# Optimization experiments

Hardware: AMD Instinct MI355X
Metric: run time of the kernel (lower is better)

Reference implementation:

```python
import math
import jax, jax.numpy as jnp
import numpy as np

# --- dimensions ---
B = 32          # crystals
N_PER = 96      # building blocks per crystal
M = B * N_PER   # total nodes = 3072
H = 8           # no_heads
CH = 16         # c_hidden
PQK = 8         # no_qk_points
PV = 12         # no_v_points
CS = 256        # c_s
CZ = 128        # c_z
E = B * N_PER * N_PER  # dense intra-crystal edges = 294912
INV_SOFTPLUS_1 = 0.541324854612918


def _quat_to_rot(q):
    """Unit quaternion [M,4] -> rotation matrices [M,3,3]."""
    w, x, y, z = q[:, 0], q[:, 1], q[:, 2], q[:, 3]
    R = jnp.stack([
        1 - 2 * (y * y + z * z), 2 * (x * y - w * z), 2 * (x * z + w * y),
        2 * (x * y + w * z), 1 - 2 * (x * x + z * z), 2 * (y * z - w * x),
        2 * (x * z - w * y), 2 * (y * z + w * x), 1 - 2 * (x * x + y * y)],
        axis=-1)
    return R.reshape(-1, 3, 3)


def _lin_params(k, din, dout):
    kw, kb = jax.random.split(k)
    W = jax.random.normal(kw, (din, dout), jnp.float32) / np.sqrt(din).astype(np.float32)
    b = jax.random.normal(kb, (dout,), jnp.float32) * 0.01
    return W, b


def setup_inputs() -> dict:
    key = jax.random.key(0)
    ks = jax.random.split(key, 16)
    s = jax.random.normal(ks[0], (M, CS), jnp.float32)
    z = jax.random.normal(ks[1], (E, CZ), jnp.float32)
    quat = jax.random.normal(ks[2], (M, 4), jnp.float32)
    rot = _quat_to_rot(quat / jnp.linalg.norm(quat, axis=-1, keepdims=True))
    trans = jax.random.normal(ks[3], (M, 3), jnp.float32)
    L = jax.random.normal(ks[4], (B, 6), jnp.float32)
    # block-diagonal fully-connected intra-crystal edges
    i = np.repeat(np.arange(N_PER), N_PER)
    j = np.tile(np.arange(N_PER), N_PER)
    off = (np.arange(B) * N_PER)[:, None]
    src = (off + i[None, :]).reshape(-1)
    tgt = (off + j[None, :]).reshape(-1)
    edge_index = jnp.asarray(np.stack([src, tgt]), jnp.int32)
    num_bbs = jnp.full((B,), N_PER, jnp.int32)
    Wq, bq = _lin_params(ks[5], CS, H * CH)
    Wkv, bkv = _lin_params(ks[6], CS, 2 * H * CH)
    Wqp, bqp = _lin_params(ks[7], CS, H * PQK * 3)
    Wkvp, bkvp = _lin_params(ks[8], CS, H * (PQK + PV) * 3)
    Wb, bb = _lin_params(ks[9], CZ, H)
    Wl, bl = _lin_params(ks[10], 6, H)
    head_weights = INV_SOFTPLUS_1 + 0.1 * jax.random.normal(ks[11], (H,), jnp.float32)
    Wout, bout = _lin_params(ks[12], H * (CH + 3 * PV) + 6, CS)
    return dict(s=s, z=z, rot=rot, trans=trans, L=L,
                Wq=Wq, bq=bq, Wkv=Wkv, bkv=bkv, Wqp=Wqp, bqp=bqp,
                Wkvp=Wkvp, bkvp=bkvp, Wb=Wb, bb=bb, Wl=Wl, bl=bl,
                head_weights=head_weights, Wout=Wout, bout=bout,
                edge_index=edge_index, num_bbs=num_bbs)


def reference(s, z, rot, trans, L, Wq, bq, Wkv, bkv, Wqp, bqp, Wkvp, bkvp,
              Wb, bb, Wl, bl, head_weights, Wout, bout, edge_index, num_bbs):
    src, tgt = edge_index[0], edge_index[1]
    # scalar q/k/v
    q = (s @ Wq + bq).reshape(M, H, CH)
    kv = (s @ Wkv + bkv).reshape(M, H, 2 * CH)
    k, v = kv[..., :CH], kv[..., CH:]

    # point q/k/v: torch splits last dim into 3 coord chunks then stacks -> reshape (M,3,H,P)
    def points(W, bias, P):
        p = (s @ W + bias).reshape(M, 3, H, P).transpose(0, 2, 3, 1)  # [M,H,P,3]
        return jnp.einsum('mij,mhpj->mhpi', rot, p) + trans[:, None, None, :]

    q_pts = points(Wqp, bqp, PQK)                 # [M,H,PQK,3] in global frame
    kv_pts = points(Wkvp, bkvp, PQK + PV)         # [M,H,PQK+PV,3]
    k_pts, v_pts = kv_pts[:, :, :PQK], kv_pts[:, :, PQK:]

    b_pair = z @ Wb + bb                          # [E,H]
    batch_idx = jnp.repeat(jnp.arange(B), num_bbs, total_repeat_length=M)  # node -> crystal
    l_nodes = (L @ Wl + bl)[batch_idx]            # [M,H]

    # fused multi-term attention logits
    a = jnp.einsum('ehc,ehc->eh', q[tgt], k[src]) * math.sqrt(1.0 / (4 * CH))
    a = a + 0.5 * b_pair + 0.5 * l_nodes[src]
    disp = q_pts[tgt] - k_pts[src]                # [E,H,PQK,3]
    pt_att = jnp.sum(disp * disp, axis=-1)        # [E,H,PQK]
    hw = jax.nn.softplus(head_weights) * math.sqrt(1.0 / (4 * (PQK * 9.0 / 2)))
    a = a - 0.5 * jnp.sum(pt_att * hw[None, :, None], axis=-1)

    # segment softmax over incoming edges of each target node
    amax = jax.ops.segment_max(a, tgt, num_segments=M)
    ex = jnp.exp(a - amax[tgt])
    denom = jax.ops.segment_sum(ex, tgt, num_segments=M)
    attn = ex / denom[tgt]                        # [E,H]

    o = jax.ops.segment_sum(attn[..., None] * v[src], tgt, num_segments=M)
    o = o.reshape(M, H * CH)
    o_pt = jax.ops.segment_sum(attn[..., None, None] * v_pts[src], tgt, num_segments=M)
    o_pt = o_pt.reshape(M, H * PV, 3)
    o_l = L[batch_idx]                            # [M,6]
    o_feats = jnp.concatenate([o, o_pt[..., 0], o_pt[..., 1], o_pt[..., 2], o_l], axis=-1)
    return o_feats @ Wout + bout                  # [M,CS]
```

## Files before the change

kernel.cpp:

```cpp
#include <hip/hip_runtime.h>
#include <math.h>

#define B_    32
#define NPER_ 96
#define M_    3072
#define H_    8
#define CH_   16
#define PQK_  8
#define PV_   12
#define CS_   256
#define CZ_   128
#define E_    294912
#define NCAT_ 1056
#define OF_   432

template <bool ALIGN_A>
__global__ __launch_bounds__(256) void gemm64(const float* __restrict__ A,
                                              const float* __restrict__ W,
                                              const float* __restrict__ bias,
                                              float* __restrict__ C,
                                              int N, int K, int KW) {
  __shared__ float As[16][68];
  __shared__ float Bs[16][64];
  const int tid = threadIdx.x;
  const int tx = tid & 15, ty = tid >> 4;
  const int row0 = blockIdx.y * 64, col0 = blockIdx.x * 64;
  float acc[4][4] = {};

  for (int k0 = 0; k0 < K; k0 += 16) {
    {
      const int m = tid >> 2, k4 = (tid & 3) * 4;
      const int gk = k0 + k4;
      float a0 = 0.f, a1 = 0.f, a2 = 0.f, a3 = 0.f;
      if (ALIGN_A) {
        const float4 av = *reinterpret_cast<const float4*>(A + (size_t)(row0 + m) * K + gk);
        a0 = av.x; a1 = av.y; a2 = av.z; a3 = av.w;
      } else {
        const float* ap = A + (size_t)(row0 + m) * K;
        if (gk + 0 < K) a0 = ap[gk + 0];
        if (gk + 1 < K) a1 = ap[gk + 1];
        if (gk + 2 < K) a2 = ap[gk + 2];
        if (gk + 3 < K) a3 = ap[gk + 3];
      }
      As[k4 + 0][m] = a0; As[k4 + 1][m] = a1; As[k4 + 2][m] = a2; As[k4 + 3][m] = a3;
    }
    {
      const int kk = tid >> 4, n4 = (tid & 15) * 4;
      const int gk = k0 + kk, gn = col0 + n4;
      float4 bv; bv.x = 0.f; bv.y = 0.f; bv.z = 0.f; bv.w = 0.f;
      if (gk < KW) {
        if (gn + 3 < N) {
          bv = *reinterpret_cast<const float4*>(W + (size_t)gk * N + gn);
        } else {
          const float* wp = W + (size_t)gk * N;
          if (gn + 0 < N) bv.x = wp[gn + 0];
          if (gn + 1 < N) bv.y = wp[gn + 1];
          if (gn + 2 < N) bv.z = wp[gn + 2];
          if (gn + 3 < N) bv.w = wp[gn + 3];
        }
      }
      *reinterpret_cast<float4*>(&Bs[kk][n4]) = bv;
    }
    __syncthreads();
#pragma unroll
    for (int kk = 0; kk < 16; ++kk) {
      const float4 a_ = *reinterpret_cast<const float4*>(&As[kk][ty * 4]);
      const float4 b_ = *reinterpret_cast<const float4*>(&Bs[kk][tx * 4]);
      acc[0][0] += a_.x * b_.x; acc[0][1] += a_.x * b_.y; acc[0][2] += a_.x * b_.z; acc[0][3] += a_.x * b_.w;
      acc[1][0] += a_.y * b_.x; acc[1][1] += a_.y * b_.y; acc[1][2] += a_.y * b_.z; acc[1][3] += a_.y * b_.w;
      acc[2][0] += a_.z * b_.x; acc[2][1] += a_.z * b_.y; acc[2][2] += a_.z * b_.z; acc[2][3] += a_.z * b_.w;
      acc[3][0] += a_.w * b_.x; acc[3][1] += a_.w * b_.y; acc[3][2] += a_.w * b_.z; acc[3][3] += a_.w * b_.w;
    }
    __syncthreads();
  }
  const int gn0 = col0 + tx * 4;
#pragma unroll
  for (int i2 = 0; i2 < 4; ++i2) {
    const int gr = row0 + ty * 4 + i2;
    if (gn0 + 3 < N) {
      const float4 bsv = *reinterpret_cast<const float4*>(bias + gn0);
      float4 cv;
      cv.x = acc[i2][0] + bsv.x; cv.y = acc[i2][1] + bsv.y;
      cv.z = acc[i2][2] + bsv.z; cv.w = acc[i2][3] + bsv.w;
      *reinterpret_cast<float4*>(C + (size_t)gr * N + gn0) = cv;
    } else {
#pragma unroll
      for (int j2 = 0; j2 < 4; ++j2) {
        const int gn = gn0 + j2;
        if (gn < N) C[(size_t)gr * N + gn] = acc[i2][j2] + bias[gn];
      }
    }
  }
}

__global__ __launch_bounds__(256) void gemm128(const float* __restrict__ A,
                                               const float* __restrict__ W,
                                               const float* __restrict__ bias,
                                               float* __restrict__ C,
                                               int N, int K) {
  __shared__ float As[16][132];
  __shared__ float Bs[16][64];
  const int tid = threadIdx.x;
  const int tx = tid & 15, ty = tid >> 4;
  const int row0 = blockIdx.y * 128, col0 = blockIdx.x * 64;
  float acc[8][4] = {};

  for (int k0 = 0; k0 < K; k0 += 16) {
#pragma unroll
    for (int u = 0; u < 2; ++u) {
      const int idx = tid * 2 + u;
      const int r = idx >> 2, c = (idx & 3) * 4;
      const float4 av = *reinterpret_cast<const float4*>(A + (size_t)(row0 + r) * K + k0 + c);
      As[c + 0][r] = av.x; As[c + 1][r] = av.y; As[c + 2][r] = av.z; As[c + 3][r] = av.w;
    }
    {
      const int kk = tid >> 4, n4 = (tid & 15) * 4;
      const int gn = col0 + n4;
      float4 bv; bv.x = 0.f; bv.y = 0.f; bv.z = 0.f; bv.w = 0.f;
      if (gn + 3 < N) {
        bv = *reinterpret_cast<const float4*>(W + (size_t)(k0 + kk) * N + gn);
      } else {
        const float* wp = W + (size_t)(k0 + kk) * N;
        if (gn + 0 < N) bv.x = wp[gn + 0];
        if (gn + 1 < N) bv.y = wp[gn + 1];
        if (gn + 2 < N) bv.z = wp[gn + 2];
        if (gn + 3 < N) bv.w = wp[gn + 3];
      }
      *reinterpret_cast<float4*>(&Bs[kk][n4]) = bv;
    }
    __syncthreads();
#pragma unroll
    for (int kk = 0; kk < 16; ++kk) {
      const float4 a0 = *reinterpret_cast<const float4*>(&As[kk][ty * 8]);
      const float4 a1 = *reinterpret_cast<const float4*>(&As[kk][ty * 8 + 4]);
      const float4 b_ = *reinterpret_cast<const float4*>(&Bs[kk][tx * 4]);
      acc[0][0] += a0.x * b_.x; acc[0][1] += a0.x * b_.y; acc[0][2] += a0.x * b_.z; acc[0][3] += a0.x * b_.w;
      acc[1][0] += a0.y * b_.x; acc[1][1] += a0.y * b_.y; acc[1][2] += a0.y * b_.z; acc[1][3] += a0.y * b_.w;
      acc[2][0] += a0.z * b_.x; acc[2][1] += a0.z * b_.y; acc[2][2] += a0.z * b_.z; acc[2][3] += a0.z * b_.w;
      acc[3][0] += a0.w * b_.x; acc[3][1] += a0.w * b_.y; acc[3][2] += a0.w * b_.z; acc[3][3] += a0.w * b_.w;
      acc[4][0] += a1.x * b_.x; acc[4][1] += a1.x * b_.y; acc[4][2] += a1.x * b_.z; acc[4][3] += a1.x * b_.w;
      acc[5][0] += a1.y * b_.x; acc[5][1] += a1.y * b_.y; acc[5][2] += a1.y * b_.z; acc[5][3] += a1.y * b_.w;
      acc[6][0] += a1.z * b_.x; acc[6][1] += a1.z * b_.y; acc[6][2] += a1.z * b_.z; acc[6][3] += a1.z * b_.w;
      acc[7][0] += a1.w * b_.x; acc[7][1] += a1.w * b_.y; acc[7][2] += a1.w * b_.z; acc[7][3] += a1.w * b_.w;
    }
    __syncthreads();
  }
  const int gn0 = col0 + tx * 4;
#pragma unroll
  for (int i2 = 0; i2 < 8; ++i2) {
    const int gr = row0 + ty * 8 + i2;
    if (gn0 + 3 < N) {
      const float4 bsv = *reinterpret_cast<const float4*>(bias + gn0);
      float4 cv;
      cv.x = acc[i2][0] + bsv.x; cv.y = acc[i2][1] + bsv.y;
      cv.z = acc[i2][2] + bsv.z; cv.w = acc[i2][3] + bsv.w;
      *reinterpret_cast<float4*>(C + (size_t)gr * N + gn0) = cv;
    } else {
#pragma unroll
      for (int j2 = 0; j2 < 4; ++j2) {
        const int gn = gn0 + j2;
        if (gn < N) C[(size_t)gr * N + gn] = acc[i2][j2] + bias[gn];
      }
    }
  }
}

__global__ __launch_bounds__(256) void pack_w(const float* __restrict__ Wq,
                                              const float* __restrict__ Wkv,
                                              const float* __restrict__ Wqp,
                                              const float* __restrict__ Wkvp,
                                              const float* __restrict__ bq,
                                              const float* __restrict__ bkv,
                                              const float* __restrict__ bqp,
                                              const float* __restrict__ bkvp,
                                              float* __restrict__ Wcat,
                                              float* __restrict__ bcat) {
  const int t = blockIdx.x * 256 + threadIdx.x;
  if (t < 256 * NCAT_) {
    const int k = t / NCAT_, n = t - k * NCAT_;
    float v;
    if (n < 128)      v = Wq [k * 128 + n];
    else if (n < 384) v = Wkv[k * 256 + n - 128];
    else if (n < 576) v = Wqp[k * 192 + n - 384];
    else              v = Wkvp[k * 480 + n - 576];
    Wcat[t] = v;
  }
  if (t < NCAT_) {
    float v;
    if (t < 128)      v = bq[t];
    else if (t < 384) v = bkv[t - 128];
    else if (t < 576) v = bqp[t - 384];
    else              v = bkvp[t - 576];
    bcat[t] = v;
  }
}

__global__ __launch_bounds__(256) void rotate_pts(const float* __restrict__ praw,
                                                  const float* __restrict__ rot,
                                                  const float* __restrict__ trans,
                                                  const float* __restrict__ L,
                                                  float* __restrict__ qpts,
                                                  float* __restrict__ kpts,
                                                  float* __restrict__ vpts,
                                                  float* __restrict__ ofeat) {
  const int m = blockIdx.x;
  const int t = threadIdx.x;
  float R[9], T[3];
#pragma unroll
  for (int a = 0; a < 9; ++a) R[a] = rot[m * 9 + a];
#pragma unroll
  for (int a = 0; a < 3; ++a) T[a] = trans[m * 3 + a];
  const float* prow = praw + (size_t)m * NCAT_;

  if (t < 64) {
    const float x = prow[384 + t];
    const float y = prow[384 + 64 + t];
    const float z = prow[384 + 128 + t];
    const int h = t >> 3, p = t & 7;
    float* dst = qpts + ((size_t)(m * 8 + h) * 8 + p) * 3;
    dst[0] = R[0] * x + R[1] * y + R[2] * z + T[0];
    dst[1] = R[3] * x + R[4] * y + R[5] * z + T[1];
    dst[2] = R[6] * x + R[7] * y + R[8] * z + T[2];
  } else if (t < 224) {
    const int idx = t - 64;
    const float x = prow[576 + idx];
    const float y = prow[576 + 160 + idx];
    const float z = prow[576 + 320 + idx];
    const int h = idx / 20, p = idx % 20;
    const float o0 = R[0] * x + R[1] * y + R[2] * z + T[0];
    const float o1 = R[3] * x + R[4] * y + R[5] * z + T[1];
    const float o2 = R[6] * x + R[7] * y + R[8] * z + T[2];
    float* dst = (p < 8) ? (kpts + ((size_t)(m * 8 + h) * 8 + p) * 3)
                         : (vpts + ((size_t)(m * 8 + h) * 12 + (p - 8)) * 3);
    dst[0] = o0; dst[1] = o1; dst[2] = o2;
  } else if (t < 230) {
    ofeat[(size_t)m * OF_ + 416 + (t - 224)] = L[(m / NPER_) * 6 + (t - 224)];
  }
}

__global__ __launch_bounds__(256) void bpair_kernel(const float* __restrict__ z,
                                                    const float* __restrict__ Wb,
                                                    const float* __restrict__ bb,
                                                    float* __restrict__ bT2) {
  __shared__ float lds_out[96 * 9];
  const int bid = blockIdx.x;
  const int b = bid / 96, i = bid - b * 96;
  const int l = threadIdx.x & 63;
  const int w = threadIdx.x >> 6;
  const float4* W4 = reinterpret_cast<const float4*>(Wb);
  const float4 w0 = W4[l * 4 + 0];
  const float4 w1 = W4[l * 4 + 1];
  const float4 w2 = W4[l * 4 + 2];
  const float4 w3 = W4[l * 4 + 3];
  const int b0 = l & 1, b1 = (l >> 1) & 1, b2 = (l >> 2) & 1;
  const int myh = (b0 << 2) | (b1 << 1) | b2;
  const float mybb = bb[myh];
  const float2* z2 = reinterpret_cast<const float2*>(z);
  const size_t e0 = (size_t)b * 9216 + (size_t)i * 96;

#pragma unroll 1
  for (int j = w; j < 96; j += 4) {
    const float2 zv = z2[(e0 + j) * 64 + l];
    float a0 = zv.x * w0.x + zv.y * w2.x;
    float a1 = zv.x * w0.y + zv.y * w2.y;
    float a2 = zv.x * w0.z + zv.y * w2.z;
    float a3 = zv.x * w0.w + zv.y * w2.w;
    float a4 = zv.x * w1.x + zv.y * w3.x;
    float a5 = zv.x * w1.y + zv.y * w3.y;
    float a6 = zv.x * w1.z + zv.y * w3.z;
    float a7 = zv.x * w1.w + zv.y * w3.w;
    float s40 = (b0 ? a4 : a0) + __shfl_xor(b0 ? a0 : a4, 1);
    float s41 = (b0 ? a5 : a1) + __shfl_xor(b0 ? a1 : a5, 1);
    float s42 = (b0 ? a6 : a2) + __shfl_xor(b0 ? a2 : a6, 1);
    float s43 = (b0 ? a7 : a3) + __shfl_xor(b0 ? a3 : a7, 1);
    float s20 = (b1 ? s42 : s40) + __shfl_xor(b1 ? s40 : s42, 2);
    float s21 = (b1 ? s43 : s41) + __shfl_xor(b1 ? s41 : s43, 2);
    float s1 = (b2 ? s21 : s20) + __shfl_xor(b2 ? s20 : s21, 4);
    s1 += __shfl_xor(s1, 8);
    s1 += __shfl_xor(s1, 16);
    s1 += __shfl_xor(s1, 32);
    if (l < 8) lds_out[j * 9 + myh] = s1 + mybb;
  }
  __syncthreads();
  for (int idx = threadIdx.x; idx < 768; idx += 256) {
    const int h = idx / 96, j = idx - h * 96;
    bT2[(size_t)h * E_ + e0 + j] = lds_out[j * 9 + h];
  }
}

__global__ __launch_bounds__(768, 3) void attn_kernel(const float* __restrict__ praw,
                                                      const float* __restrict__ qpts,
                                                      const float* __restrict__ kpts,
                                                      const float* __restrict__ vpts,
                                                      const float* __restrict__ bT2,
                                                      const float* __restrict__ L,
                                                      const float* __restrict__ Wl,
                                                      const float* __restrict__ bl,
                                                      const float* __restrict__ hwts,
                                                      float* __restrict__ ofeat) {
  const int b = blockIdx.x >> 3, h = blockIdx.x & 7;
  __shared__ float4 k4[96 * 5];
  __shared__ float4 v4[96 * 5];
  __shared__ float4 kp4[96 * 6];
  __shared__ float4 vp4[96 * 9];
  __shared__ float lds_b[96 * 100];
  const int tid = threadIdx.x;

  {
    const int i = tid >> 3, c = tid & 7;
    const float4* src = reinterpret_cast<const float4*>(praw + (size_t)(b * 96 + i) * NCAT_ + 128 + h * 32);
    if (c < 4) k4[i * 5 + c] = src[c];
    else       v4[i * 5 + (c - 4)] = src[c];
  }
  for (int t = tid; t < 96 * 6; t += 768) {
    const int i = t / 6, c = t - i * 6;
    kp4[t] = reinterpret_cast<const float4*>(kpts + ((size_t)(b * 96 + i) * 8 + h) * 24)[c];
  }
  for (int t = tid; t < 96 * 9; t += 768) {
    const int i = t / 9, c = t - i * 9;
    vp4[t] = reinterpret_cast<const float4*>(vpts + ((size_t)(b * 96 + i) * 8 + h) * 36)[c];
  }
  {
    const float4* g4 = reinterpret_cast<const float4*>(bT2 + (size_t)h * E_ + (size_t)b * 9216);
    for (int t = tid; t < 2304; t += 768) {
      const int ii = t / 24, c = t - ii * 24;
      reinterpret_cast<float4*>(lds_b + ii * 100)[c] = g4[t];
    }
  }
  __syncthreads();

  const int j = tid >> 3, qq = tid & 7;
  const int mj = b * 96 + j;

  float lb = bl[h];
#pragma unroll
  for (int d = 0; d < 6; ++d) lb += L[b * 6 + d] * Wl[d * 8 + h];
  const float c_l = 0.5f * lb;
  const float sp = logf(1.0f + __expf(hwts[h]));
  const float c_pt = 0.5f * sp * (1.0f / 12.0f);

  const float4* q4 = reinterpret_cast<const float4*>(praw + (size_t)mj * NCAT_ + h * 16);
  const float4 qa = q4[0], qb = q4[1], qc = q4[2], qd = q4[3];
  float qp[24];
  {
    const float4* qp4 = reinterpret_cast<const float4*>(qpts + ((size_t)mj * 8 + h) * 24);
#pragma unroll
    for (int c4 = 0; c4 < 6; ++c4) {
      const float4 v_ = qp4[c4];
      qp[c4 * 4 + 0] = v_.x; qp[c4 * 4 + 1] = v_.y; qp[c4 * 4 + 2] = v_.z; qp[c4 * 4 + 3] = v_.w;
    }
  }

  float lg[12];
  float mx = -3.0e38f;
#pragma unroll
  for (int s = 0; s < 12; ++s) {
    const int i = s * 8 + qq;
    const float4 ka = k4[i * 5 + 0], kb = k4[i * 5 + 1], kc = k4[i * 5 + 2], kd = k4[i * 5 + 3];
    float dot = qa.x * ka.x + qa.y * ka.y + qa.z * ka.z + qa.w * ka.w
              + qb.x * kb.x + qb.y * kb.y + qb.z * kb.z + qb.w * kb.w
              + qc.x * kc.x + qc.y * kc.y + qc.z * kc.z + qc.w * kc.w
              + qd.x * kd.x + qd.y * kd.y + qd.z * kd.z + qd.w * kd.w;
    float pd = 0.f;
#pragma unroll
    for (int c4 = 0; c4 < 6; ++c4) {
      const float4 kp = kp4[i * 6 + c4];
      const float d0 = qp[c4 * 4 + 0] - kp.x;
      const float d1 = qp[c4 * 4 + 1] - kp.y;
      const float d2 = qp[c4 * 4 + 2] - kp.z;
      const float d3 = qp[c4 * 4 + 3] - kp.w;
      pd += d0 * d0 + d1 * d1 + d2 * d2 + d3 * d3;
    }
    const float lv = dot * 0.125f + 0.5f * lds_b[i * 100 + j] + c_l - c_pt * pd;
    lg[s] = lv;
    mx = fmaxf(mx, lv);
  }
  mx = fmaxf(mx, __shfl_xor(mx, 1));
  mx = fmaxf(mx, __shfl_xor(mx, 2));
  mx = fmaxf(mx, __shfl_xor(mx, 4));
  float sum = 0.f;
#pragma unroll
  for (int s = 0; s < 12; ++s) { lg[s] = __expf(lg[s] - mx); sum += lg[s]; }
  sum += __shfl_xor(sum, 1);
  sum += __shfl_xor(sum, 2);
  sum += __shfl_xor(sum, 4);
  const float inv = 1.0f / sum;

  float acco[16] = {};
  float accp[36] = {};
#pragma unroll
  for (int s = 0; s < 12; ++s) {
    const int i = s * 8 + qq;
    const float w = lg[s];
#pragma unroll
    for (int c4 = 0; c4 < 4; ++c4) {
      const float4 vv = v4[i * 5 + c4];
      acco[c4 * 4 + 0] += w * vv.x; acco[c4 * 4 + 1] += w * vv.y;
      acco[c4 * 4 + 2] += w * vv.z; acco[c4 * 4 + 3] += w * vv.w;
    }
#pragma unroll
    for (int c4 = 0; c4 < 9; ++c4) {
      const float4 pv = vp4[i * 9 + c4];
      accp[c4 * 4 + 0] += w * pv.x; accp[c4 * 4 + 1] += w * pv.y;
      accp[c4 * 4 + 2] += w * pv.z; accp[c4 * 4 + 3] += w * pv.w;
    }
  }
#pragma unroll
  for (int u = 0; u < 16; ++u) {
    acco[u] += __shfl_xor(acco[u], 1); acco[u] += __shfl_xor(acco[u], 2); acco[u] += __shfl_xor(acco[u], 4);
  }
#pragma unroll
  for (int u = 0; u < 36; ++u) {
    accp[u] += __shfl_xor(accp[u], 1); accp[u] += __shfl_xor(accp[u], 2); accp[u] += __shfl_xor(accp[u], 4);
  }

  if (qq == 0) {
    float* orow = ofeat + (size_t)mj * OF_;
#pragma unroll
    for (int c = 0; c < 16; ++c) orow[h * 16 + c] = acco[c] * inv;
#pragma unroll
    for (int d = 0; d < 3; ++d)
#pragma unroll
      for (int p = 0; p < 12; ++p)
        orow[128 + d * 96 + h * 12 + p] = accp[p * 3 + d] * inv;
  }
}

extern "C" void kernel_launch(void* const* d_in, const int* in_sizes, int n_in,
                              void* d_out, int out_size, void* d_ws, size_t ws_size,
                              hipStream_t stream) {
  const float* s     = (const float*)d_in[0];
  const float* z     = (const float*)d_in[1];
  const float* rot   = (const float*)d_in[2];
  const float* trans = (const float*)d_in[3];
  const float* L     = (const float*)d_in[4];
  const float* Wq    = (const float*)d_in[5];
  const float* bq    = (const float*)d_in[6];
  const float* Wkv   = (const float*)d_in[7];
  const float* bkv   = (const float*)d_in[8];
  const float* Wqp   = (const float*)d_in[9];
  const float* bqp   = (const float*)d_in[10];
  const float* Wkvp  = (const float*)d_in[11];
  const float* bkvp  = (const float*)d_in[12];
  const float* Wb    = (const float*)d_in[13];
  const float* bb    = (const float*)d_in[14];
  const float* Wl    = (const float*)d_in[15];
  const float* bl    = (const float*)d_in[16];
  const float* hwts  = (const float*)d_in[17];
  const float* Wout  = (const float*)d_in[18];
  const float* bout  = (const float*)d_in[19];
  float* out = (float*)d_out;
  float* ws  = (float*)d_ws;

  float* praw  = ws;
  float* qpts  = praw  + 3244032;
  float* kpts  = qpts  + 589824;
  float* vpts  = kpts  + 589824;
  float* ofeat = vpts  + 884736;
  float* bT2   = ofeat + 1327104;
  float* Wcat  = bT2   + 2359296;
  float* bcat  = Wcat  + 270336;

  pack_w<<<(256 * NCAT_ + 255) / 256, 256, 0, stream>>>(Wq, Wkv, Wqp, Wkvp, bq, bkv, bqp, bkvp, Wcat, bcat);
  gemm128<<<dim3(17, 24), 256, 0, stream>>>(s, Wcat, bcat, praw, NCAT_, 256);
  rotate_pts<<<M_, 256, 0, stream>>>(praw, rot, trans, L, qpts, kpts, vpts, ofeat);
  bpair_kernel<<<M_, 256, 0, stream>>>(z, Wb, bb, bT2);
  attn_kernel<<<256, 768, 0, stream>>>(praw, qpts, kpts, vpts, bT2, L, Wl, bl, hwts, ofeat);
  gemm64<true ><<<dim3(4, 48), 256, 0, stream>>>(ofeat, Wout, bout, out, 256, OF_, 422);
}
```

Measured before the change: 387.4 us.

## Fuse projection GEMM and pair-bias kernel into one launch, drop weight packing

Removes the separate weight-concatenation kernel by having the projection GEMM read directly from the four source weight matrices, chosen per column tile. The projection GEMM (now 64x64 tiles) and the pair-bias reduction over z are merged into a single launch with block-index dispatch, so the small GEMM can run alongside the bandwidth-heavy z pass. This saves two launches and the Wcat write/read, at the cost of smaller GEMM tiles and shared memory sized for the larger of the two branches.

```diff
diff --git a/kernel.cpp b/kernel.cpp
--- a/kernel.cpp
+++ b/kernel.cpp
@@ -13,6 +13,7 @@
 #define E_    294912
 #define NCAT_ 1056
 #define OF_   432
+#define GEMM_BLOCKS 816
 
 template <bool ALIGN_A>
 __global__ __launch_bounds__(256) void gemm64(const float* __restrict__ A,
@@ -93,105 +94,120 @@
   }
 }
 
-__global__ __launch_bounds__(256) void gemm128(const float* __restrict__ A,
-                                               const float* __restrict__ W,
-                                               const float* __restrict__ bias,
-                                               float* __restrict__ C,
-                                               int N, int K) {
-  __shared__ float As[16][132];
-  __shared__ float Bs[16][64];
+__global__ __launch_bounds__(256) void proj_bpair(const float* __restrict__ s,
+                                                  const float* __restrict__ Wq,
+                                                  const float* __restrict__ Wkv,
+                                                  const float* __restrict__ Wqp,
+                                                  const float* __restrict__ Wkvp,
+                                                  const float* __restrict__ bq,
+                                                  const float* __restrict__ bkv,
+                                                  const float* __restrict__ bqp,
+                                                  const float* __restrict__ bkvp,
+                                                  const float* __restrict__ z,
+                                                  const float* __restrict__ Wb,
+                                                  const float* __restrict__ bb,
+                                                  float* __restrict__ praw,
+                                                  float* __restrict__ bT2) {
+  __shared__ float smem[16 * 68 + 16 * 64];
+  const int bid = blockIdx.x;
   const int tid = threadIdx.x;
-  const int tx = tid & 15, ty = tid >> 4;
-  const int row0 = blockIdx.y * 128, col0 = blockIdx.x * 64;
-  float acc[8][4] = {};
-
-  for (int k0 = 0; k0 < K; k0 += 16) {
-#pragma unroll
-    for (int u = 0; u < 2; ++u) {
-      const int idx = tid * 2 + u;
-      const int r = idx >> 2, c = (idx & 3) * 4;
-      const float4 av = *reinterpret_cast<const float4*>(A + (size_t)(row0 + r) * K + k0 + c);
-      As[c + 0][r] = av.x; As[c + 1][r] = av.y; As[c + 2][r] = av.z; As[c + 3][r] = av.w;
-    }
-    {
-      const int kk = tid >> 4, n4 = (tid & 15) * 4;
-      const int gn = col0 + n4;
-      float4 bv; bv.x = 0.f; bv.y = 0.f; bv.z = 0.f; bv.w = 0.f;
-      if (gn + 3 < N) {
-        bv = *reinterpret_cast<const float4*>(W + (size_t)(k0 + kk) * N + gn);
-      } else {
-        const float* wp = W + (size_t)(k0 + kk) * N;
-        if (gn + 0 < N) bv.x = wp[gn + 0];
-        if (gn + 1 < N) bv.y = wp[gn + 1];
-        if (gn + 2 < N) bv.z = wp[gn + 2];
-        if (gn + 3 < N) bv.w = wp[gn + 3];
-      }
-      *reinterpret_cast<float4*>(&Bs[kk][n4]) = bv;
+
+  if (bid < GEMM_BLOCKS) {
+    float (*As)[68] = reinterpret_cast<float(*)[68]>(smem);
+    float (*Bs)[64] = reinterpret_cast<float(*)[64]>(smem + 16 * 68);
+    const int cb = bid % 17, rb = bid / 17;
+    const int row0 = rb * 64, col0 = cb * 64;
+    const float* Wsrc; const float* bsrc; int Nsrc, cbase;
+    if (col0 < 128)      { Wsrc = Wq;   bsrc = bq;   Nsrc = 128; cbase = 0; }
+    else if (col0 < 384) { Wsrc = Wkv;  bsrc = bkv;  Nsrc = 256; cbase = 128; }
+    else if (col0 < 576) { Wsrc = Wqp;  bsrc = bqp;  Nsrc = 192; cbase = 384; }
+    else                 { Wsrc = Wkvp; bsrc = bkvp; Nsrc = 480; cbase = 576; }
+    const int csrc0 = col0 - cbase;
+    const int tx = tid & 15, ty = tid >> 4;
+    float acc[4][4] = {};
+
+    for (int k0 = 0; k0 < 256; k0 += 16) {
+      {
+        const int m = tid >> 2, k4 = (tid & 3) * 4;
+        const float4 av = *reinterpret_cast<const float4*>(s + (size_t)(row0 + m) * 256 + k0 + k4);
+        As[k4 + 0][m] = av.x; As[k4 + 1][m] = av.y; As[k4 + 2][m] = av.z; As[k4 + 3][m] = av.w;
+      }
+      {
+        const int kk = tid >> 4, n4 = (tid & 15) * 4;
+        const int gnl = csrc0 + n4;
+        float4 bv; bv.x = 0.f; bv.y = 0.f; bv.z = 0.f; bv.w = 0.f;
+        if (gnl < Nsrc) bv = *reinterpret_cast<const float4*>(Wsrc + (size_t)(k0 + kk) * Nsrc + gnl);
+        *reinterpret_cast<float4*>(&Bs[kk][n4]) = bv;
+      }
+      __syncthreads();
+#pragma unroll
+      for (int kk = 0; kk < 16; ++kk) {
+        const float4 a_ = *reinterpret_cast<const float4*>(&As[kk][ty * 4]);
+        const float4 b_ = *reinterpret_cast<const float4*>(&Bs[kk][tx * 4]);
+        acc[0][0] += a_.x * b_.x; acc[0][1] += a_.x * b_.y; acc[0][2] += a_.x * b_.z; acc[0][3] += a_.x * b_.w;
+        acc[1][0] += a_.y * b_.x; acc[1][1] += a_.y * b_.y; acc[1][2] += a_.y * b_.z; acc[1][3] += a_.y * b_.w;
+        acc[2][0] += a_.z * b_.x; acc[2][1] += a_.z * b_.y; acc[2][2] += a_.z * b_.z; acc[2][3] += a_.z * b_.w;
+        acc[3][0] += a_.w * b_.x; acc[3][1] += a_.w * b_.y; acc[3][2] += a_.w * b_.z; acc[3][3] += a_.w * b_.w;
+      }
+      __syncthreads();
+    }
+    const int gnl0 = csrc0 + tx * 4;
+    if (gnl0 < Nsrc) {
+      const float4 bsv = *reinterpret_cast<const float4*>(bsrc + gnl0);
+#pragma unroll
+      for (int i2 = 0; i2 < 4; ++i2) {
+        const int gr = row0 + ty * 4 + i2;
+        float4 cv;
+        cv.x = acc[i2][0] + bsv.x; cv.y = acc[i2][1] + bsv.y;
+        cv.z = acc[i2][2] + bsv.z; cv.w = acc[i2][3] + bsv.w;
+        *reinterpret_cast<float4*>(praw + (size_t)gr * NCAT_ + col0 + tx * 4) = cv;
+      }
+    }
+  } else {
+    float* lds_out = smem;
+    const int eb = bid - GEMM_BLOCKS;
+    const int b = eb / 96, i = eb - b * 96;
+    const int l = tid & 63;
+    const int w = tid >> 6;
+    const float4* W4 = reinterpret_cast<const float4*>(Wb);
+    const float4 w0 = W4[l * 4 + 0];
+    const float4 w1 = W4[l * 4 + 1];
+    const float4 w2 = W4[l * 4 + 2];
+    const float4 w3 = W4[l * 4 + 3];
+    const int b0 = l & 1, b1 = (l >> 1) & 1, b2 = (l >> 2) & 1;
+    const int myh = (b0 << 2) | (b1 << 1) | b2;
+    const float mybb = bb[myh];
+    const float2* z2 = reinterpret_cast<const float2*>(z);
+    const size_t e0 = (size_t)b * 9216 + (size_t)i * 96;
+
+#pragma unroll 1
+    for (int j = w; j < 96; j += 4) {
+      const float2 zv = z2[(e0 + j) * 64 + l];
+      float a0 = zv.x * w0.x + zv.y * w2.x;
+      float a1 = zv.x * w0.y + zv.y * w2.y;
+      float a2 = zv.x * w0.z + zv.y * w2.z;
+      float a3 = zv.x * w0.w + zv.y * w2.w;
+      float a4 = zv.x * w1.x + zv.y * w3.x;
+      float a5 = zv.x * w1.y + zv.y * w3.y;
+      float a6 = zv.x * w1.z + zv.y * w3.z;
+      float a7 = zv.x * w1.w + zv.y * w3.w;
+      float s40 = (b0 ? a4 : a0) + __shfl_xor(b0 ? a0 : a4, 1);
+      float s41 = (b0 ? a5 : a1) + __shfl_xor(b0 ? a1 : a5, 1);
+      float s42 = (b0 ? a6 : a2) + __shfl_xor(b0 ? a2 : a6, 1);
+      float s43 = (b0 ? a7 : a3) + __shfl_xor(b0 ? a3 : a7, 1);
+      float s20 = (b1 ? s42 : s40) + __shfl_xor(b1 ? s40 : s42, 2);
+      float s21 = (b1 ? s43 : s41) + __shfl_xor(b1 ? s41 : s43, 2);
+      float s1 = (b2 ? s21 : s20) + __shfl_xor(b2 ? s20 : s21, 4);
+      s1 += __shfl_xor(s1, 8);
+      s1 += __shfl_xor(s1, 16);
+      s1 += __shfl_xor(s1, 32);
+      if (l < 8) lds_out[j * 9 + myh] = s1 + mybb;
     }
     __syncthreads();
-#pragma unroll
-    for (int kk = 0; kk < 16; ++kk) {
-      const float4 a0 = *reinterpret_cast<const float4*>(&As[kk][ty * 8]);
-      const float4 a1 = *reinterpret_cast<const float4*>(&As[kk][ty * 8 + 4]);
-      const float4 b_ = *reinterpret_cast<const float4*>(&Bs[kk][tx * 4]);
-      acc[0][0] += a0.x * b_.x; acc[0][1] += a0.x * b_.y; acc[0][2] += a0.x * b_.z; acc[0][3] += a0.x * b_.w;
-      acc[1][0] += a0.y * b_.x; acc[1][1] += a0.y * b_.y; acc[1][2] += a0.y * b_.z; acc[1][3] += a0.y * b_.w;
-      acc[2][0] += a0.z * b_.x; acc[2][1] += a0.z * b_.y; acc[2][2] += a0.z * b_.z; acc[2][3] += a0.z * b_.w;
-      acc[3][0] += a0.w * b_.x; acc[3][1] += a0.w * b_.y; acc[3][2] += a0.w * b_.z; acc[3][3] += a0.w * b_.w;
-      acc[4][0] += a1.x * b_.x; acc[4][1] += a1.x * b_.y; acc[4][2] += a1.x * b_.z; acc[4][3] += a1.x * b_.w;
-      acc[5][0] += a1.y * b_.x; acc[5][1] += a1.y * b_.y; acc[5][2] += a1.y * b_.z; acc[5][3] += a1.y * b_.w;
-      acc[6][0] += a1.z * b_.x; acc[6][1] += a1.z * b_.y; acc[6][2] += a1.z * b_.z; acc[6][3] += a1.z * b_.w;
-      acc[7][0] += a1.w * b_.x; acc[7][1] += a1.w * b_.y; acc[7][2] += a1.w * b_.z; acc[7][3] += a1.w * b_.w;
-    }
-    __syncthreads();
-  }
-  const int gn0 = col0 + tx * 4;
-#pragma unroll
-  for (int i2 = 0; i2 < 8; ++i2) {
-    const int gr = row0 + ty * 8 + i2;
-    if (gn0 + 3 < N) {
-      const float4 bsv = *reinterpret_cast<const float4*>(bias + gn0);
-      float4 cv;
-      cv.x = acc[i2][0] + bsv.x; cv.y = acc[i2][1] + bsv.y;
-      cv.z = acc[i2][2] + bsv.z; cv.w = acc[i2][3] + bsv.w;
-      *reinterpret_cast<float4*>(C + (size_t)gr * N + gn0) = cv;
-    } else {
-#pragma unroll
-      for (int j2 = 0; j2 < 4; ++j2) {
-        const int gn = gn0 + j2;
-        if (gn < N) C[(size_t)gr * N + gn] = acc[i2][j2] + bias[gn];
-      }
-    }
-  }
-}
-
-__global__ __launch_bounds__(256) void pack_w(const float* __restrict__ Wq,
-                                              const float* __restrict__ Wkv,
-                                              const float* __restrict__ Wqp,
-                                              const float* __restrict__ Wkvp,
-                                              const float* __restrict__ bq,
-                                              const float* __restrict__ bkv,
-                                              const float* __restrict__ bqp,
-                                              const float* __restrict__ bkvp,
-                                              float* __restrict__ Wcat,
-                                              float* __restrict__ bcat) {
-  const int t = blockIdx.x * 256 + threadIdx.x;
-  if (t < 256 * NCAT_) {
-    const int k = t / NCAT_, n = t - k * NCAT_;
-    float v;
-    if (n < 128)      v = Wq [k * 128 + n];
-    else if (n < 384) v = Wkv[k * 256 + n - 128];
-    else if (n < 576) v = Wqp[k * 192 + n - 384];
-    else              v = Wkvp[k * 480 + n - 576];
-    Wcat[t] = v;
-  }
-  if (t < NCAT_) {
-    float v;
-    if (t < 128)      v = bq[t];
-    else if (t < 384) v = bkv[t - 128];
-    else if (t < 576) v = bqp[t - 384];
-    else              v = bkvp[t - 576];
-    bcat[t] = v;
+    for (int idx = tid; idx < 768; idx += 256) {
+      const int h = idx / 96, j = idx - h * 96;
+      bT2[(size_t)h * E_ + e0 + j] = lds_out[j * 9 + h];
+    }
   }
 }
 
@@ -235,56 +251,6 @@
     dst[0] = o0; dst[1] = o1; dst[2] = o2;
   } else if (t < 230) {
     ofeat[(size_t)m * OF_ + 416 + (t - 224)] = L[(m / NPER_) * 6 + (t - 224)];
-  }
-}
-
-__global__ __launch_bounds__(256) void bpair_kernel(const float* __restrict__ z,
-                                                    const float* __restrict__ Wb,
-                                                    const float* __restrict__ bb,
-                                                    float* __restrict__ bT2) {
-  __shared__ float lds_out[96 * 9];
-  const int bid = blockIdx.x;
-  const int b = bid / 96, i = bid - b * 96;
-  const int l = threadIdx.x & 63;
-  const int w = threadIdx.x >> 6;
-  const float4* W4 = reinterpret_cast<const float4*>(Wb);
-  const float4 w0 = W4[l * 4 + 0];
-  const float4 w1 = W4[l * 4 + 1];
-  const float4 w2 = W4[l * 4 + 2];
-  const float4 w3 = W4[l * 4 + 3];
-  const int b0 = l & 1, b1 = (l >> 1) & 1, b2 = (l >> 2) & 1;
-  const int myh = (b0 << 2) | (b1 << 1) | b2;
-  const float mybb = bb[myh];
-  const float2* z2 = reinterpret_cast<const float2*>(z);
-  const size_t e0 = (size_t)b * 9216 + (size_t)i * 96;
-
-#pragma unroll 1
-  for (int j = w; j < 96; j += 4) {
-    const float2 zv = z2[(e0 + j) * 64 + l];
-    float a0 = zv.x * w0.x + zv.y * w2.x;
-    float a1 = zv.x * w0.y + zv.y * w2.y;
-    float a2 = zv.x * w0.z + zv.y * w2.z;
-    float a3 = zv.x * w0.w + zv.y * w2.w;
-    float a4 = zv.x * w1.x + zv.y * w3.x;
-    float a5 = zv.x * w1.y + zv.y * w3.y;
-    float a6 = zv.x * w1.z + zv.y * w3.z;
-    float a7 = zv.x * w1.w + zv.y * w3.w;
-    float s40 = (b0 ? a4 : a0) + __shfl_xor(b0 ? a0 : a4, 1);
-    float s41 = (b0 ? a5 : a1) + __shfl_xor(b0 ? a1 : a5, 1);
-    float s42 = (b0 ? a6 : a2) + __shfl_xor(b0 ? a2 : a6, 1);
-    float s43 = (b0 ? a7 : a3) + __shfl_xor(b0 ? a3 : a7, 1);
-    float s20 = (b1 ? s42 : s40) + __shfl_xor(b1 ? s40 : s42, 2);
-    float s21 = (b1 ? s43 : s41) + __shfl_xor(b1 ? s41 : s43, 2);
-    float s1 = (b2 ? s21 : s20) + __shfl_xor(b2 ? s20 : s21, 4);
-    s1 += __shfl_xor(s1, 8);
-    s1 += __shfl_xor(s1, 16);
-    s1 += __shfl_xor(s1, 32);
-    if (l < 8) lds_out[j * 9 + myh] = s1 + mybb;
-  }
-  __syncthreads();
-  for (int idx = threadIdx.x; idx < 768; idx += 256) {
-    const int h = idx / 96, j = idx - h * 96;
-    bT2[(size_t)h * E_ + e0 + j] = lds_out[j * 9 + h];
   }
 }
 
@@ -458,13 +424,11 @@
   float* vpts  = kpts  + 589824;
   float* ofeat = vpts  + 884736;
   float* bT2   = ofeat + 1327104;
-  float* Wcat  = bT2   + 2359296;
-  float* bcat  = Wcat  + 270336;
-
-  pack_w<<<(256 * NCAT_ + 255) / 256, 256, 0, stream>>>(Wq, Wkv, Wqp, Wkvp, bq, bkv, bqp, bkvp, Wcat, bcat);
-  gemm128<<<dim3(17, 24), 256, 0, stream>>>(s, Wcat, bcat, praw, NCAT_, 256);
+
+  proj_bpair<<<GEMM_BLOCKS + M_, 256, 0, stream>>>(s, Wq, Wkv, Wqp, Wkvp,
+                                                   bq, bkv, bqp, bkvp,
+                                                   z, Wb, bb, praw, bT2);
   rotate_pts<<<M_, 256, 0, stream>>>(praw, rot, trans, L, qpts, kpts, vpts, ofeat);
-  bpair_kernel<<<M_, 256, 0, stream>>>(z, Wb, bb, bT2);
   attn_kernel<<<256, 768, 0, stream>>>(praw, qpts, kpts, vpts, bT2, L, Wl, bl, hwts, ofeat);
   gemm64<true ><<<dim3(4, 48), 256, 0, stream>>>(ofeat, Wout, bout, out, 256, OF_, 422);
 }
```

Result: faster. 366.8 us (-5.3%).
